# Performance work log

Hardware: AMD Instinct MI355X
Metric: run time of the kernel (lower is better)

The kernel has to match this reference:

```python
import jax, jax.numpy as jnp
import numpy as np

B, C, H, W = 8, 256, 48, 48
CK = 64  # C // k
WSCALE = 0.3 / np.sqrt(C)  # keep exp(QK^T) finite (original has no 1/sqrt(d) scaling)


def conv1x1(x, w, b):
    # x: (B,C,H,W), w: (O,C,1,1), b: (O,) -> (B,O,H,W)
    return jnp.einsum('bchw,oc->bohw', x, w[:, :, 0, 0]) + b[None, :, None, None]


def setup_inputs() -> dict:
    key = jax.random.key(0)
    ks = jax.random.split(key, 6)
    x = jax.random.normal(ks[0], (B, C, H, W), dtype=jnp.float32)
    qw = jax.random.normal(ks[1], (CK, C, 1, 1), dtype=jnp.float32) * WSCALE
    kw = jax.random.normal(ks[2], (CK, C, 1, 1), dtype=jnp.float32) * WSCALE
    vw = jax.random.normal(ks[3], (C, C, 1, 1), dtype=jnp.float32) * (1.0 / np.sqrt(C))
    gw = jax.random.normal(ks[4], (C, C, 1, 1), dtype=jnp.float32) * (1.0 / np.sqrt(C))
    zk = jnp.zeros((CK,), dtype=jnp.float32)
    zc = jnp.zeros((C,), dtype=jnp.float32)
    return {
        'x': x,
        'query_weight': qw, 'query_bias': zk,
        'key_weight': kw, 'key_bias': zk,
        'value_weight': vw, 'value_bias': zc,
        'gamma_weight': gw, 'gamma_bias': zc,
        'k': 4,
    }


def reference(x, query_weight, query_bias, key_weight, key_bias,
              value_weight, value_bias, gamma_weight, gamma_bias, k):
    b, c, h, w = x.shape
    n = h * w
    q = conv1x1(x, query_weight, query_bias).reshape(b, -1, n)   # (B,Ck,N)
    kk = conv1x1(x, key_weight, key_bias).reshape(b, -1, n)      # (B,Ck,N)
    # energy[b,i,j] = q_i . k_j  (queries on rows, no sqrt(d) scaling)
    energy = jnp.einsum('bci,bcj->bij', q, kk)                   # (B,N,N)
    energy = jnp.exp(energy)
    energy = energy / jnp.sum(energy, axis=2, keepdims=True)     # unnormalized-softmax over keys
    v = conv1x1(x, value_weight, value_bias).reshape(b, c, n)    # (B,C,N)
    # out[b,c,j] = sum_i v[b,c,i] * energy[b,i,j]  (faithful to torch.bmm(V, energy))
    out = jnp.einsum('bci,bij->bcj', v, energy).reshape(b, c, h, w)
    out = conv1x1(out, gamma_weight, gamma_bias)
    return out
```

## Files before the change

### kernel.cpp

```cpp
#include <hip/hip_runtime.h>

#define BATCH 8
#define CIN   256
#define NPIX  2304
#define CKD   64
#define QKLD  128
#define KSPL  3
#define KLEN  (NPIX / KSPL)

typedef _Float16 f16;
typedef __attribute__((ext_vector_type(4))) _Float16 f16x4;
typedef __attribute__((ext_vector_type(8))) _Float16 f16x8;
typedef __attribute__((ext_vector_type(4))) float    f32x4;

__global__ __launch_bounds__(256) void cast_w(
    const float* __restrict__ qw, const float* __restrict__ kw,
    const float* __restrict__ vw, const float* __restrict__ gw,
    f16* __restrict__ Wqk, f16* __restrict__ Wv, f16* __restrict__ Wg)
{
    int idx = (blockIdx.x * 256 + threadIdx.x) * 4;
    const float* src;
    f16* dst;
    if (idx < 16384)      { src = qw + idx;           dst = Wqk + idx; }
    else if (idx < 32768) { src = kw + (idx - 16384); dst = Wqk + idx; }
    else if (idx < 98304) { src = vw + (idx - 32768); dst = Wv + (idx - 32768); }
    else                  { src = gw + (idx - 98304); dst = Wg + (idx - 98304); }
    float4 v = *(const float4*)src;
    f16x4 h = { (f16)v.x, (f16)v.y, (f16)v.z, (f16)v.w };
    *(f16x4*)dst = h;
}

__global__ __launch_bounds__(256) void cast_xT(
    const float* __restrict__ x, f16* __restrict__ xT)
{
    __shared__ float s[64][65];
    const int t = threadIdx.x;
    const int n0 = blockIdx.x * 64, c0 = blockIdx.y * 64, b = blockIdx.z;
    const float* xb = x + ((size_t)b * CIN + c0) * NPIX + n0;

    const int cl = t >> 4, ng = (t & 15) * 4;
    #pragma unroll
    for (int p = 0; p < 4; ++p) {
        float4 v = *(const float4*)(xb + (size_t)(cl + 16 * p) * NPIX + ng);
        s[cl + 16 * p][ng + 0] = v.x;
        s[cl + 16 * p][ng + 1] = v.y;
        s[cl + 16 * p][ng + 2] = v.z;
        s[cl + 16 * p][ng + 3] = v.w;
    }
    __syncthreads();
    const int nl = t >> 2, cs = (t & 3) * 16;
    f16 h[16];
    #pragma unroll
    for (int j = 0; j < 16; ++j) h[j] = (f16)s[cs + j][nl];
    f16* gp = &xT[((size_t)b * NPIX + n0 + nl) * CIN + c0 + cs];
    *(f16x8*)gp       = *(f16x8*)&h[0];
    *(f16x8*)(gp + 8) = *(f16x8*)&h[8];
}

__global__ __launch_bounds__(256) void qk_conv_mfma(
    const f16* __restrict__ xT, const f16* __restrict__ Wqk,
    const float* __restrict__ qbias, const float* __restrict__ kbias,
    f16* __restrict__ qkT)
{
    const int t = threadIdx.x, w = t >> 6, lane = t & 63;
    const int quad = lane >> 4, l16 = lane & 15;
    const int wm = w & 1, wn = w >> 1;
    const int n0 = blockIdx.x * 32, b = blockIdx.y;

    const f16* bp = xT + ((size_t)b * NPIX + n0 + 16 * wn + l16) * CIN;
    const f16* ap = Wqk + (size_t)(64 * wm + l16) * CIN;

    f32x4 acc[4];
    #pragma unroll
    for (int mt = 0; mt < 4; ++mt) acc[mt] = (f32x4){0.f, 0.f, 0.f, 0.f};

    #pragma unroll
    for (int kk = 0; kk < CIN; kk += 32) {
        f16x8 bf = *(const f16x8*)(bp + kk + quad * 8);
        #pragma unroll
        for (int mt = 0; mt < 4; ++mt) {
            f16x8 af = *(const f16x8*)(ap + (size_t)mt * 16 * CIN + kk + quad * 8);
            acc[mt] = __builtin_amdgcn_mfma_f32_16x16x32_f16(af, bf, acc[mt], 0, 0, 0);
        }
    }
    const int n = n0 + 16 * wn + l16;
    const float* bias = wm ? kbias - 64 : qbias;
    #pragma unroll
    for (int mt = 0; mt < 4; ++mt) {
        int ob = 64 * wm + 16 * mt + quad * 4;
        f16x4 h;
        #pragma unroll
        for (int r = 0; r < 4; ++r)
            h[r] = (f16)(acc[mt][r] + bias[ob + r]);
        *(f16x4*)&qkT[((size_t)b * NPIX + n) * QKLD + ob] = h;
    }
}

__global__ __launch_bounds__(256) void energy_mfma(
    const f16* __restrict__ qkT, float* __restrict__ S, f16* __restrict__ Et)
{
    __shared__ f16   es[64][72];
    __shared__ float red2[4][64];
    const int t    = threadIdx.x;
    const int w    = t >> 6, lane = t & 63;
    const int quad = lane >> 4, l16 = lane & 15;
    const int j0 = blockIdx.x * 64, i0 = blockIdx.y * 64, b = blockIdx.z;
    const f16* base = qkT + (size_t)b * NPIX * QKLD;

    f32x4 acc[4];
    #pragma unroll
    for (int mt = 0; mt < 4; ++mt) acc[mt] = (f32x4){0.f, 0.f, 0.f, 0.f};

    #pragma unroll
    for (int ks = 0; ks < 2; ++ks) {
        f16x8 bf = *(const f16x8*)&base[(size_t)(j0 + 16 * w + l16) * QKLD + 64 + ks * 32 + quad * 8];
        #pragma unroll
        for (int mt = 0; mt < 4; ++mt) {
            f16x8 af = *(const f16x8*)&base[(size_t)(i0 + 16 * mt + l16) * QKLD + ks * 32 + quad * 8];
            acc[mt] = __builtin_amdgcn_mfma_f32_16x16x32_f16(af, bf, acc[mt], 0, 0, 0);
        }
    }

    #pragma unroll
    for (int mt = 0; mt < 4; ++mt) {
        f16x4 h = { (f16)__expf(acc[mt][0]), (f16)__expf(acc[mt][1]),
                    (f16)__expf(acc[mt][2]), (f16)__expf(acc[mt][3]) };
        *(f16x4*)&es[16 * w + l16][16 * mt + quad * 4] = h;
    }
    __syncthreads();

    {
        int j = t >> 2, ch = (t & 3) * 16;
        f16x8 v0 = *(const f16x8*)&es[j][ch];
        f16x8 v1 = *(const f16x8*)&es[j][ch + 8];
        f16* gp = &Et[((size_t)b * NPIX + j0 + j) * NPIX + i0 + ch];
        *(f16x8*)gp       = v0;
        *(f16x8*)(gp + 8) = v1;
    }
    {
        int i = t & 63, jq = t >> 6;
        float s = 0.f;
        #pragma unroll
        for (int jj = 0; jj < 16; ++jj)
            s += (float)es[jq * 16 + jj][i];
        red2[jq][i] = s;
    }
    __syncthreads();
    if (t < 64) {
        float s = red2[0][t] + red2[1][t] + red2[2][t] + red2[3][t];
        atomicAdd(&S[(size_t)b * NPIX + i0 + t], s);
    }
}

__global__ __launch_bounds__(256) void v_conv_mfma(
    const f16* __restrict__ xT, const f16* __restrict__ Wv,
    const float* __restrict__ vbias, const float* __restrict__ S,
    f16* __restrict__ u)
{
    __shared__ __align__(16) f16 As[128 * 40];
    __shared__ __align__(16) f16 Bs[64 * 40];
    const int t = threadIdx.x, w = t >> 6, lane = t & 63;
    const int quad = lane >> 4, l16 = lane & 15;
    const int wm = w & 1, wn = w >> 1;
    const int i0 = blockIdx.x * 64, c0 = blockIdx.y * 128, b = blockIdx.z;
    const int sub = t >> 2, le = t & 3;
    const f16* srcA = Wv + (size_t)(c0 + sub) * CIN + le * 8;
    const f16* srcB = xT + ((size_t)b * NPIX + i0 + sub) * CIN + le * 8;
    const int ldsw = sub * 40 + le * 8;

    f32x4 acc[4][2];
    #pragma unroll
    for (int mt = 0; mt < 4; ++mt)
        #pragma unroll
        for (int nt = 0; nt < 2; ++nt)
            acc[mt][nt] = (f32x4){0.f, 0.f, 0.f, 0.f};

    for (int kk = 0; kk < CIN; kk += 32) {
        f16x8 ta0 = *(const f16x8*)(srcA + kk);
        f16x8 ta1 = *(const f16x8*)(srcA + (size_t)64 * CIN + kk);
        f16x8 tb0 = *(const f16x8*)(srcB + kk);
        __syncthreads();
        *(f16x8*)&As[ldsw]           = ta0;
        *(f16x8*)&As[64 * 40 + ldsw] = ta1;
        *(f16x8*)&Bs[ldsw]           = tb0;
        __syncthreads();
        f16x8 af[4], bf[2];
        #pragma unroll
        for (int mt = 0; mt < 4; ++mt)
            af[mt] = *(const f16x8*)&As[(64 * wm + 16 * mt + l16) * 40 + quad * 8];
        #pragma unroll
        for (int nt = 0; nt < 2; ++nt)
            bf[nt] = *(const f16x8*)&Bs[(32 * wn + 16 * nt + l16) * 40 + quad * 8];
        #pragma unroll
        for (int mt = 0; mt < 4; ++mt)
            #pragma unroll
            for (int nt = 0; nt < 2; ++nt)
                acc[mt][nt] = __builtin_amdgcn_mfma_f32_16x16x32_f16(
                    af[mt], bf[nt], acc[mt][nt], 0, 0, 0);
    }

    #pragma unroll
    for (int nt = 0; nt < 2; ++nt) {
        int i = i0 + 32 * wn + 16 * nt + l16;
        float is = 1.0f / S[(size_t)b * NPIX + i];
        #pragma unroll
        for (int mt = 0; mt < 4; ++mt)
            #pragma unroll
            for (int r = 0; r < 4; ++r) {
                int c = c0 + 64 * wm + 16 * mt + quad * 4 + r;
                u[((size_t)b * CIN + c) * NPIX + i] =
                    (f16)((acc[mt][nt][r] + vbias[c]) * is);
            }
    }
}

__global__ __launch_bounds__(512, 2) void bmm_mfma(
    const f16* __restrict__ u, const f16* __restrict__ Et,
    f16* __restrict__ p0, f16* __restrict__ p1, f16* __restrict__ p2)
{
    __shared__ __align__(16) f16 As[256 * 32];
    __shared__ __align__(16) f16 Bs[128 * 32];
    const int t = threadIdx.x, w = t >> 6, lane = t & 63;
    const int quad = lane >> 4, l16 = lane & 15;
    const int wc = w & 3, wj = w >> 2;
    const int j0 = blockIdx.x * 128;
    const int ks = blockIdx.y, b = blockIdx.z;
    const int kb = ks * KLEN;
    const f16* ub = u  + (size_t)b * CIN * NPIX;
    const f16* eb = Et + (size_t)b * NPIX * NPIX;
    f16* outp = (ks == 0) ? p0 : (ks == 1 ? p1 : p2);

    const int rA  = t >> 2;
    const int chp = t & 3;
    const int chd = chp ^ ((t >> 3) & 3);
    const f16* srcA0 = ub + (size_t)rA * NPIX + kb + chd * 8;
    const f16* srcA1 = srcA0 + (size_t)128 * NPIX;
    const f16* srcB  = eb + (size_t)(j0 + rA) * NPIX + kb + chd * 8;
    const int ldsA0 = rA * 32 + chp * 8;
    const int ldsA1 = (rA + 128) * 32 + chp * 8;
    const int ldsB  = rA * 32 + chp * 8;
    const int swz = (quad ^ ((l16 >> 1) & 3)) * 8;

    f32x4 acc[4][4];
    #pragma unroll
    for (int mt = 0; mt < 4; ++mt)
        #pragma unroll
        for (int nt = 0; nt < 4; ++nt)
            acc[mt][nt] = (f32x4){0.f, 0.f, 0.f, 0.f};

    for (int kk = 0; kk < KLEN; kk += 32) {
        f16x8 ta0 = *(const f16x8*)(srcA0 + kk);
        f16x8 ta1 = *(const f16x8*)(srcA1 + kk);
        f16x8 tb0 = *(const f16x8*)(srcB + kk);
        __syncthreads();
        *(f16x8*)&As[ldsA0] = ta0;
        *(f16x8*)&As[ldsA1] = ta1;
        *(f16x8*)&Bs[ldsB]  = tb0;
        __syncthreads();
        f16x8 af[4], bf[4];
        #pragma unroll
        for (int mt = 0; mt < 4; ++mt)
            af[mt] = *(const f16x8*)&As[(64 * wc + 16 * mt + l16) * 32 + swz];
        #pragma unroll
        for (int nt = 0; nt < 4; ++nt)
            bf[nt] = *(const f16x8*)&Bs[(64 * wj + 16 * nt + l16) * 32 + swz];
        #pragma unroll
        for (int mt = 0; mt < 4; ++mt)
            #pragma unroll
            for (int nt = 0; nt < 4; ++nt)
                acc[mt][nt] = __builtin_amdgcn_mfma_f32_16x16x32_f16(
                    af[mt], bf[nt], acc[mt][nt], 0, 0, 0);
    }

    #pragma unroll
    for (int mt = 0; mt < 4; ++mt) {
        int cb = 64 * wc + 16 * mt + quad * 4;
        #pragma unroll
        for (int nt = 0; nt < 4; ++nt) {
            int j = j0 + 64 * wj + 16 * nt + l16;
            f16x4 h = { (f16)acc[mt][nt][0], (f16)acc[mt][nt][1],
                        (f16)acc[mt][nt][2], (f16)acc[mt][nt][3] };
            *(f16x4*)&outp[((size_t)b * NPIX + j) * CIN + cb] = h;
        }
    }
}

__global__ __launch_bounds__(256) void gamma_conv_mfma(
    const f16* __restrict__ p0, const f16* __restrict__ p1,
    const f16* __restrict__ p2, const f16* __restrict__ Wg,
    const float* __restrict__ gbias, float* __restrict__ out)
{
    __shared__ __align__(16) f16 As[128 * 40];
    __shared__ __align__(16) f16 Bs[64 * 40];
    const int t = threadIdx.x, w = t >> 6, lane = t & 63;
    const int quad = lane >> 4, l16 = lane & 15;
    const int wm = w & 1, wn = w >> 1;
    const int j0 = blockIdx.x * 64, o0 = blockIdx.y * 128, b = blockIdx.z;
    const int sub = t >> 2, le = t & 3;
    const f16* srcA  = Wg + (size_t)(o0 + sub) * CIN + le * 8;
    const size_t boff = ((size_t)b * NPIX + j0 + sub) * CIN + le * 8;
    const int ldsw = sub * 40 + le * 8;

    f32x4 acc[4][2];
    #pragma unroll
    for (int mt = 0; mt < 4; ++mt)
        #pragma unroll
        for (int nt = 0; nt < 2; ++nt)
            acc[mt][nt] = (f32x4){0.f, 0.f, 0.f, 0.f};

    for (int kk = 0; kk < CIN; kk += 32) {
        f16x8 ta0 = *(const f16x8*)(srcA + kk);
        f16x8 ta1 = *(const f16x8*)(srcA + (size_t)64 * CIN + kk);
        f16x8 tb0 = *(const f16x8*)(p0 + boff + kk);
        f16x8 tb1 = *(const f16x8*)(p1 + boff + kk);
        f16x8 tb2 = *(const f16x8*)(p2 + boff + kk);
        f16x8 tbs = tb0 + tb1 + tb2;
        __syncthreads();
        *(f16x8*)&As[ldsw]           = ta0;
        *(f16x8*)&As[64 * 40 + ldsw] = ta1;
        *(f16x8*)&Bs[ldsw]           = tbs;
        __syncthreads();
        f16x8 af[4], bf[2];
        #pragma unroll
        for (int mt = 0; mt < 4; ++mt)
            af[mt] = *(const f16x8*)&As[(64 * wm + 16 * mt + l16) * 40 + quad * 8];
        #pragma unroll
        for (int nt = 0; nt < 2; ++nt)
            bf[nt] = *(const f16x8*)&Bs[(32 * wn + 16 * nt + l16) * 40 + quad * 8];
        #pragma unroll
        for (int mt = 0; mt < 4; ++mt)
            #pragma unroll
            for (int nt = 0; nt < 2; ++nt)
                acc[mt][nt] = __builtin_amdgcn_mfma_f32_16x16x32_f16(
                    af[mt], bf[nt], acc[mt][nt], 0, 0, 0);
    }

    #pragma unroll
    for (int mt = 0; mt < 4; ++mt)
        #pragma unroll
        for (int r = 0; r < 4; ++r) {
            int o = o0 + 64 * wm + 16 * mt + quad * 4 + r;
            float bv = gbias[o];
            #pragma unroll
            for (int nt = 0; nt < 2; ++nt) {
                int j = j0 + 32 * wn + 16 * nt + l16;
                out[((size_t)b * CIN + o) * NPIX + j] = acc[mt][nt][r] + bv;
            }
        }
}

extern "C" void kernel_launch(void* const* d_in, const int* in_sizes, int n_in,
                              void* d_out, int out_size, void* d_ws, size_t ws_size,
                              hipStream_t stream) {
    const float* x   = (const float*)d_in[0];
    const float* qw  = (const float*)d_in[1];
    const float* qbv = (const float*)d_in[2];
    const float* kw  = (const float*)d_in[3];
    const float* kbv = (const float*)d_in[4];
    const float* vw  = (const float*)d_in[5];
    const float* vbv = (const float*)d_in[6];
    const float* gw  = (const float*)d_in[7];
    const float* gbv = (const float*)d_in[8];
    float* out = (float*)d_out;

    const size_t BCN  = (size_t)BATCH * CIN * NPIX;
    const size_t BN   = (size_t)BATCH * NPIX;
    const size_t BNN  = (size_t)BATCH * NPIX * NPIX;
    const size_t BNQK = (size_t)BATCH * NPIX * QKLD;

    f16* Et   = (f16*)d_ws;
    f16* u    = Et + BNN;
    f16* xT   = u + BCN;
    f16* qkT  = xT + BCN;
    f16* p1   = qkT + BNQK;
    f16* p2   = p1 + BCN;
    f16* Wqk  = p2 + BCN;
    f16* Wv   = Wqk + 128 * 256;
    f16* Wg   = Wv + 256 * 256;
    float* S  = (float*)(Wg + 256 * 256);
    f16* p0   = xT;

    hipMemsetAsync(S, 0, BN * sizeof(float), stream);

    cast_w<<<160, 256, 0, stream>>>(qw, kw, vw, gw, Wqk, Wv, Wg);
    cast_xT<<<dim3(NPIX / 64, CIN / 64, BATCH), 256, 0, stream>>>(x, xT);
    qk_conv_mfma<<<dim3(NPIX / 32, BATCH), 256, 0, stream>>>(xT, Wqk, qbv, kbv, qkT);
    energy_mfma<<<dim3(NPIX / 64, NPIX / 64, BATCH), 256, 0, stream>>>(qkT, S, Et);
    v_conv_mfma<<<dim3(NPIX / 64, CIN / 128, BATCH), 256, 0, stream>>>(xT, Wv, vbv, S, u);
    bmm_mfma<<<dim3(NPIX / 128, KSPL, BATCH), 512, 0, stream>>>(u, Et, p0, p1, p2);
    gamma_conv_mfma<<<dim3(NPIX / 64, CIN / 128, BATCH), 256, 0, stream>>>(p0, p1, p2, Wg, gbv, out);
}
```

Measured before the change: 225.4 us.

## Store energy and values in MFMA fragment layout; drop LDS staging in bmm

Energy and scaled-value tensors are now written in a pre-blocked layout that matches the MFMA operand fragments, so each lane of the bmm kernel loads its operand directly from global memory and the LDS staging and barriers go away. Energy tiles grow to 128 rows, and row sums are written as per-block partials and summed by a new reduce_S kernel instead of atomics plus a memset. The K-split in bmm rises from 3 to 4, which adds one more partial buffer for the gamma conv to sum. The cost is an extra kernel launch, more partial-output traffic, and bmm reading global memory without LDS reuse across waves.

```diff
diff --git a/kernel.cpp b/kernel.cpp
--- a/kernel.cpp
+++ b/kernel.cpp
@@ -5,8 +5,11 @@
 #define NPIX  2304
 #define CKD   64
 #define QKLD  128
-#define KSPL  3
-#define KLEN  (NPIX / KSPL)
+#define NJT   (NPIX / 16)
+#define NIC   (NPIX / 32)
+#define KSPL  4
+#define ICPS  (NIC / KSPL)
+#define NJB   (NPIX / 64)
 
 typedef _Float16 f16;
 typedef __attribute__((ext_vector_type(4))) _Float16 f16x4;
@@ -96,69 +99,87 @@
     }
 }
 
+#define ESL 136
 __global__ __launch_bounds__(256) void energy_mfma(
-    const f16* __restrict__ qkT, float* __restrict__ S, f16* __restrict__ Et)
-{
-    __shared__ f16   es[64][72];
-    __shared__ float red2[4][64];
+    const f16* __restrict__ qkT, float* __restrict__ Pred,
+    f16* __restrict__ Et_blk)
+{
+    __shared__ __align__(16) f16 es[64 * ESL];
+    __shared__ float red2[2][128];
     const int t    = threadIdx.x;
     const int w    = t >> 6, lane = t & 63;
     const int quad = lane >> 4, l16 = lane & 15;
-    const int j0 = blockIdx.x * 64, i0 = blockIdx.y * 64, b = blockIdx.z;
+    const int j0 = blockIdx.x * 64, i0 = blockIdx.y * 128, b = blockIdx.z;
     const f16* base = qkT + (size_t)b * NPIX * QKLD;
 
-    f32x4 acc[4];
-    #pragma unroll
-    for (int mt = 0; mt < 4; ++mt) acc[mt] = (f32x4){0.f, 0.f, 0.f, 0.f};
+    f32x4 acc[8];
+    #pragma unroll
+    for (int mt = 0; mt < 8; ++mt) acc[mt] = (f32x4){0.f, 0.f, 0.f, 0.f};
 
     #pragma unroll
     for (int ks = 0; ks < 2; ++ks) {
         f16x8 bf = *(const f16x8*)&base[(size_t)(j0 + 16 * w + l16) * QKLD + 64 + ks * 32 + quad * 8];
         #pragma unroll
-        for (int mt = 0; mt < 4; ++mt) {
+        for (int mt = 0; mt < 8; ++mt) {
             f16x8 af = *(const f16x8*)&base[(size_t)(i0 + 16 * mt + l16) * QKLD + ks * 32 + quad * 8];
             acc[mt] = __builtin_amdgcn_mfma_f32_16x16x32_f16(af, bf, acc[mt], 0, 0, 0);
         }
     }
 
     #pragma unroll
-    for (int mt = 0; mt < 4; ++mt) {
+    for (int mt = 0; mt < 8; ++mt) {
         f16x4 h = { (f16)__expf(acc[mt][0]), (f16)__expf(acc[mt][1]),
                     (f16)__expf(acc[mt][2]), (f16)__expf(acc[mt][3]) };
-        *(f16x4*)&es[16 * w + l16][16 * mt + quad * 4] = h;
+        *(f16x4*)&es[(16 * w + l16) * ESL + 16 * mt + quad * 4] = h;
     }
     __syncthreads();
 
+    #pragma unroll
+    for (int p = 0; p < 4; ++p) {
+        int g  = t + 256 * p;
+        int jt = g >> 8, ic = (g >> 6) & 3, ln = g & 63;
+        f16x8 v = *(const f16x8*)&es[(jt * 16 + (ln & 15)) * ESL + ic * 32 + (ln >> 4) * 8];
+        *(f16x8*)&Et_blk[(((size_t)b * NJT + (j0 >> 4) + jt) * NIC + (i0 >> 5) + ic) * 512 + ln * 8] = v;
+    }
+
     {
-        int j = t >> 2, ch = (t & 3) * 16;
-        f16x8 v0 = *(const f16x8*)&es[j][ch];
-        f16x8 v1 = *(const f16x8*)&es[j][ch + 8];
-        f16* gp = &Et[((size_t)b * NPIX + j0 + j) * NPIX + i0 + ch];
-        *(f16x8*)gp       = v0;
-        *(f16x8*)(gp + 8) = v1;
-    }
-    {
-        int i = t & 63, jq = t >> 6;
+        int i = t & 127, jq = t >> 7;
         float s = 0.f;
         #pragma unroll
-        for (int jj = 0; jj < 16; ++jj)
-            s += (float)es[jq * 16 + jj][i];
+        for (int jj = 0; jj < 32; ++jj)
+            s += (float)es[(jq * 32 + jj) * ESL + i];
         red2[jq][i] = s;
     }
     __syncthreads();
-    if (t < 64) {
-        float s = red2[0][t] + red2[1][t] + red2[2][t] + red2[3][t];
-        atomicAdd(&S[(size_t)b * NPIX + i0 + t], s);
-    }
+    if (t < 128) {
+        Pred[((size_t)b * NPIX + i0 + t) * NJB + blockIdx.x] =
+            red2[0][t] + red2[1][t];
+    }
+}
+
+__global__ __launch_bounds__(256) void reduce_S(
+    const float* __restrict__ Pred, float* __restrict__ S)
+{
+    int idx = blockIdx.x * 256 + threadIdx.x;
+    const float* p = Pred + (size_t)idx * NJB;
+    float s = 0.f;
+    #pragma unroll
+    for (int x = 0; x < NJB; x += 4) {
+        float4 v = *(const float4*)(p + x);
+        s += v.x + v.y + v.z + v.w;
+    }
+    S[idx] = s;
 }
 
 __global__ __launch_bounds__(256) void v_conv_mfma(
     const f16* __restrict__ xT, const f16* __restrict__ Wv,
     const float* __restrict__ vbias, const float* __restrict__ S,
-    f16* __restrict__ u)
-{
-    __shared__ __align__(16) f16 As[128 * 40];
-    __shared__ __align__(16) f16 Bs[64 * 40];
+    f16* __restrict__ u_blk)
+{
+    __shared__ __align__(16) f16 smem[9216];
+    f16* As = smem;
+    f16* Bs = smem + 128 * 40;
+    f16* us = smem;
     const int t = threadIdx.x, w = t >> 6, lane = t & 63;
     const int quad = lane >> 4, l16 = lane & 15;
     const int wm = w & 1, wn = w >> 1;
@@ -199,47 +220,43 @@
                     af[mt], bf[nt], acc[mt][nt], 0, 0, 0);
     }
 
+    __syncthreads();
     #pragma unroll
     for (int nt = 0; nt < 2; ++nt) {
-        int i = i0 + 32 * wn + 16 * nt + l16;
-        float is = 1.0f / S[(size_t)b * NPIX + i];
+        int i = 32 * wn + 16 * nt + l16;
+        float is = 1.0f / S[(size_t)b * NPIX + i0 + i];
         #pragma unroll
         for (int mt = 0; mt < 4; ++mt)
             #pragma unroll
             for (int r = 0; r < 4; ++r) {
-                int c = c0 + 64 * wm + 16 * mt + quad * 4 + r;
-                u[((size_t)b * CIN + c) * NPIX + i] =
-                    (f16)((acc[mt][nt][r] + vbias[c]) * is);
+                int c = 64 * wm + 16 * mt + quad * 4 + r;
+                us[c * 72 + i] = (f16)((acc[mt][nt][r] + vbias[c0 + c]) * is);
             }
     }
-}
-
-__global__ __launch_bounds__(512, 2) void bmm_mfma(
-    const f16* __restrict__ u, const f16* __restrict__ Et,
-    f16* __restrict__ p0, f16* __restrict__ p1, f16* __restrict__ p2)
-{
-    __shared__ __align__(16) f16 As[256 * 32];
-    __shared__ __align__(16) f16 Bs[128 * 32];
+    __syncthreads();
+    #pragma unroll
+    for (int p = 0; p < 4; ++p) {
+        int g  = t + 256 * p;
+        int ct = g >> 7, ic = (g >> 6) & 1, ln = g & 63;
+        f16x8 v = *(const f16x8*)&us[(ct * 16 + (ln & 15)) * 72 + ic * 32 + (ln >> 4) * 8];
+        *(f16x8*)&u_blk[(((size_t)b * 16 + (c0 >> 4) + ct) * NIC + (i0 >> 5) + ic) * 512 + ln * 8] = v;
+    }
+}
+
+__global__ __launch_bounds__(512) void bmm_mfma(
+    const f16* __restrict__ u_blk, const f16* __restrict__ Et_blk,
+    f16* __restrict__ p0, f16* __restrict__ p1,
+    f16* __restrict__ p2, f16* __restrict__ p3)
+{
     const int t = threadIdx.x, w = t >> 6, lane = t & 63;
     const int quad = lane >> 4, l16 = lane & 15;
     const int wc = w & 3, wj = w >> 2;
     const int j0 = blockIdx.x * 128;
     const int ks = blockIdx.y, b = blockIdx.z;
-    const int kb = ks * KLEN;
-    const f16* ub = u  + (size_t)b * CIN * NPIX;
-    const f16* eb = Et + (size_t)b * NPIX * NPIX;
-    f16* outp = (ks == 0) ? p0 : (ks == 1 ? p1 : p2);
-
-    const int rA  = t >> 2;
-    const int chp = t & 3;
-    const int chd = chp ^ ((t >> 3) & 3);
-    const f16* srcA0 = ub + (size_t)rA * NPIX + kb + chd * 8;
-    const f16* srcA1 = srcA0 + (size_t)128 * NPIX;
-    const f16* srcB  = eb + (size_t)(j0 + rA) * NPIX + kb + chd * 8;
-    const int ldsA0 = rA * 32 + chp * 8;
-    const int ldsA1 = (rA + 128) * 32 + chp * 8;
-    const int ldsB  = rA * 32 + chp * 8;
-    const int swz = (quad ^ ((l16 >> 1) & 3)) * 8;
+    const f16* ub  = u_blk  + (size_t)b * 16 * NIC * 512 + (size_t)lane * 8;
+    const f16* ebb = Et_blk + (size_t)b * NJT * NIC * 512 + (size_t)lane * 8;
+    f16* outp = (ks == 0) ? p0 : (ks == 1 ? p1 : (ks == 2 ? p2 : p3));
+    const int jtb = (j0 >> 4) + wj * 4;
 
     f32x4 acc[4][4];
     #pragma unroll
@@ -248,22 +265,16 @@
         for (int nt = 0; nt < 4; ++nt)
             acc[mt][nt] = (f32x4){0.f, 0.f, 0.f, 0.f};
 
-    for (int kk = 0; kk < KLEN; kk += 32) {
-        f16x8 ta0 = *(const f16x8*)(srcA0 + kk);
-        f16x8 ta1 = *(const f16x8*)(srcA1 + kk);
-        f16x8 tb0 = *(const f16x8*)(srcB + kk);
-        __syncthreads();
-        *(f16x8*)&As[ldsA0] = ta0;
-        *(f16x8*)&As[ldsA1] = ta1;
-        *(f16x8*)&Bs[ldsB]  = tb0;
-        __syncthreads();
+    const int ic0 = ks * ICPS;
+    #pragma unroll 2
+    for (int ic = ic0; ic < ic0 + ICPS; ++ic) {
         f16x8 af[4], bf[4];
         #pragma unroll
         for (int mt = 0; mt < 4; ++mt)
-            af[mt] = *(const f16x8*)&As[(64 * wc + 16 * mt + l16) * 32 + swz];
+            af[mt] = *(const f16x8*)(ub + (size_t)((wc * 4 + mt) * NIC + ic) * 512);
         #pragma unroll
         for (int nt = 0; nt < 4; ++nt)
-            bf[nt] = *(const f16x8*)&Bs[(64 * wj + 16 * nt + l16) * 32 + swz];
+            bf[nt] = *(const f16x8*)(ebb + (size_t)((jtb + nt) * NIC + ic) * 512);
         #pragma unroll
         for (int mt = 0; mt < 4; ++mt)
             #pragma unroll
@@ -274,10 +285,10 @@
 
     #pragma unroll
     for (int mt = 0; mt < 4; ++mt) {
-        int cb = 64 * wc + 16 * mt + quad * 4;
+        int cb = (wc * 4 + mt) * 16 + quad * 4;
         #pragma unroll
         for (int nt = 0; nt < 4; ++nt) {
-            int j = j0 + 64 * wj + 16 * nt + l16;
+            int j = j0 + (wj * 4 + nt) * 16 + l16;
             f16x4 h = { (f16)acc[mt][nt][0], (f16)acc[mt][nt][1],
                         (f16)acc[mt][nt][2], (f16)acc[mt][nt][3] };
             *(f16x4*)&outp[((size_t)b * NPIX + j) * CIN + cb] = h;
@@ -287,8 +298,9 @@
 
 __global__ __launch_bounds__(256) void gamma_conv_mfma(
     const f16* __restrict__ p0, const f16* __restrict__ p1,
-    const f16* __restrict__ p2, const f16* __restrict__ Wg,
-    const float* __restrict__ gbias, float* __restrict__ out)
+    const f16* __restrict__ p2, const f16* __restrict__ p3,
+    const f16* __restrict__ Wg, const float* __restrict__ gbias,
+    float* __restrict__ out)
 {
     __shared__ __align__(16) f16 As[128 * 40];
     __shared__ __align__(16) f16 Bs[64 * 40];
@@ -314,7 +326,8 @@
         f16x8 tb0 = *(const f16x8*)(p0 + boff + kk);
         f16x8 tb1 = *(const f16x8*)(p1 + boff + kk);
         f16x8 tb2 = *(const f16x8*)(p2 + boff + kk);
-        f16x8 tbs = tb0 + tb1 + tb2;
+        f16x8 tb3 = *(const f16x8*)(p3 + boff + kk);
+        f16x8 tbs = (tb0 + tb1) + (tb2 + tb3);
         __syncthreads();
         *(f16x8*)&As[ldsw]           = ta0;
         *(f16x8*)&As[64 * 40 + ldsw] = ta1;
@@ -368,25 +381,26 @@
     const size_t BNN  = (size_t)BATCH * NPIX * NPIX;
     const size_t BNQK = (size_t)BATCH * NPIX * QKLD;
 
-    f16* Et   = (f16*)d_ws;
-    f16* u    = Et + BNN;
-    f16* xT   = u + BCN;
-    f16* qkT  = xT + BCN;
-    f16* p1   = qkT + BNQK;
-    f16* p2   = p1 + BCN;
-    f16* Wqk  = p2 + BCN;
-    f16* Wv   = Wqk + 128 * 256;
-    f16* Wg   = Wv + 256 * 256;
-    float* S  = (float*)(Wg + 256 * 256);
-    f16* p0   = xT;
-
-    hipMemsetAsync(S, 0, BN * sizeof(float), stream);
+    f16* Et    = (f16*)d_ws;
+    f16* u_blk = Et + BNN;
+    f16* xT    = u_blk + BCN;
+    f16* qkT   = xT + BCN;
+    f16* p1    = qkT + BNQK;
+    f16* p2    = p1 + BCN;
+    f16* p3    = p2 + BCN;
+    f16* Wqk   = p3 + BCN;
+    f16* Wv    = Wqk + 128 * 256;
+    f16* Wg    = Wv + 256 * 256;
+    float* S   = (float*)(Wg + 256 * 256);
+    float* Pred= S + BN;
+    f16* p0    = xT;
 
     cast_w<<<160, 256, 0, stream>>>(qw, kw, vw, gw, Wqk, Wv, Wg);
     cast_xT<<<dim3(NPIX / 64, CIN / 64, BATCH), 256, 0, stream>>>(x, xT);
     qk_conv_mfma<<<dim3(NPIX / 32, BATCH), 256, 0, stream>>>(xT, Wqk, qbv, kbv, qkT);
-    energy_mfma<<<dim3(NPIX / 64, NPIX / 64, BATCH), 256, 0, stream>>>(qkT, S, Et);
-    v_conv_mfma<<<dim3(NPIX / 64, CIN / 128, BATCH), 256, 0, stream>>>(xT, Wv, vbv, S, u);
-    bmm_mfma<<<dim3(NPIX / 128, KSPL, BATCH), 512, 0, stream>>>(u, Et, p0, p1, p2);
-    gamma_conv_mfma<<<dim3(NPIX / 64, CIN / 128, BATCH), 256, 0, stream>>>(p0, p1, p2, Wg, gbv, out);
-}
+    energy_mfma<<<dim3(NPIX / 64, NPIX / 128, BATCH), 256, 0, stream>>>(qkT, Pred, Et);
+    reduce_S<<<(int)(BN / 256), 256, 0, stream>>>(Pred, S);
+    v_conv_mfma<<<dim3(NPIX / 64, CIN / 128, BATCH), 256, 0, stream>>>(xT, Wv, vbv, S, u_blk);
+    bmm_mfma<<<dim3(NPIX / 128, KSPL, BATCH), 512, 0, stream>>>(u_blk, Et, p0, p1, p2, p3);
+    gamma_conv_mfma<<<dim3(NPIX / 64, CIN / 128, BATCH), 256, 0, stream>>>(p0, p1, p2, p3, Wg, gbv, out);
+}
```

Result: no change. 228.9 us (+1.6%).
